# Optimization experiments

Measured on AMD Instinct MI355X. Metric: run time of the kernel, lower is better.

## Reference

```python
import jax, jax.numpy as jnp
import numpy as np

B, T, C = 2, 2048, 1024
H, GAMMA = 16, 8
D = C // H
SCALE = 1.0 / np.sqrt(D).astype(np.float32)


def setup_inputs() -> dict:
    key = jax.random.key(0)
    ks = jax.random.split(key, 6)
    w = 0.02
    return {
        'x': jax.random.normal(ks[0], (B, T, C), dtype=jnp.float32),
        'Wq': jax.random.normal(ks[1], (C, 2 * C), dtype=jnp.float32) * w,
        'Wk': jax.random.normal(ks[2], (C, 2 * C), dtype=jnp.float32) * w,
        'Wv': jax.random.normal(ks[3], (C, C), dtype=jnp.float32) * w,
        'Wo': jax.random.normal(ks[4], (C, C), dtype=jnp.float32) * w,
        'theta_offset': jax.random.normal(ks[5], (H,), dtype=jnp.float32) * 0.1,
    }


def _heads(t):
    # (B, T, C) -> (B, H, T, D)
    return t.reshape(B, T, H, D).transpose(0, 2, 1, 3)


def reference(x, Wq, Wk, Wv, Wo, theta_offset):
    q_raw = x @ Wq                      # (B, T, 2C)
    k_raw = x @ Wk                      # (B, T, 2C)
    v = _heads(x @ Wv)                  # (B, H, T, D)

    q_amp, q_phase = jnp.split(q_raw, 2, axis=-1)
    k_amp, k_phase = jnp.split(k_raw, 2, axis=-1)
    q_amp = jax.nn.softplus(_heads(q_amp))
    q_phase = _heads(q_phase)
    k_amp = jax.nn.softplus(_heads(k_amp))
    k_phase = _heads(k_phase)

    q_real = q_amp * jnp.cos(q_phase)
    q_imag = q_amp * jnp.sin(q_phase)
    k_real = k_amp * jnp.cos(k_phase)
    k_imag = k_amp * jnp.sin(k_phase)

    scores = (jnp.einsum('bhtd,bhsd->bhts', q_real, k_real)
              + jnp.einsum('bhtd,bhsd->bhts', q_imag, k_imag)) * SCALE

    # theta gating (active since T > GAMMA)
    cycle_ids = jnp.arange(T, dtype=jnp.float32) / GAMMA
    cycle_dist = cycle_ids[None, :] - cycle_ids[:, None]        # (T, T)
    theta_gate = jnp.cos(theta_offset[:, None, None] * cycle_dist)  # (H, T, T)
    scores = scores * theta_gate[None]

    causal = jnp.tril(jnp.ones((T, T), dtype=bool))
    scores = jnp.where(causal[None, None], scores, -jnp.inf)
    attn = jax.nn.softmax(scores, axis=-1)

    out = jnp.einsum('bhts,bhsd->bhtd', attn, v)
    out = out.transpose(0, 2, 1, 3).reshape(B, T, C)
    return out @ Wo
```

## Files before the change

### kernel.cpp

```cpp
#include <hip/hip_runtime.h>
#include <hip/hip_bf16.h>
#include <math.h>

#define Bc 2
#define Tc 2048
#define Cc 1024
#define Hc 16
#define Dc 64

typedef __attribute__((ext_vector_type(8))) short short8;
typedef __attribute__((ext_vector_type(4))) float f32x4;

#define L2E 1.44269504088896f
#define SM_M 20.0f

__device__ __forceinline__ short f2bf(float x) {
    unsigned u = __float_as_uint(x);
    u += 0x7fff + ((u >> 16) & 1);
    return (short)(u >> 16);
}
__device__ __forceinline__ unsigned pack2bf_fast(float a, float b) {
    unsigned ua = __float_as_uint(a) + 0x8000u;
    unsigned ub = __float_as_uint(b) + 0x8000u;
    return __builtin_amdgcn_perm(ub, ua, 0x07060302);
}
__device__ __forceinline__ float softplus_fast(float a) {
    return fmaxf(a, 0.f) + __logf(1.f + __expf(-fabsf(a)));
}

#define RDA(BUF, MH) do {                                                      \
    const short* Ah_ = &Al[BUF][MH][0];                                        \
    _Pragma("unroll") for (int mt_ = 0; mt_ < 4; ++mt_) {                      \
        af[mt_][0] = *(const short8*)&Ah_[(wm*64 + mt_*16 + c)*64 + rsw0];     \
        af[mt_][1] = *(const short8*)&Ah_[(wm*64 + mt_*16 + c)*64 + rsw1];     \
    } } while (0)

#define RDB(BUF, NH) do {                                                      \
    const short* Bh_ = &Bl[BUF][NH][0];                                        \
    _Pragma("unroll") for (int nf_ = 0; nf_ < 2; ++nf_) {                      \
        bfr[NH][nf_][0] = *(const short8*)&Bh_[(wn*32 + nf_*16 + c)*64 + rsw0];\
        bfr[NH][nf_][1] = *(const short8*)&Bh_[(wn*32 + nf_*16 + c)*64 + rsw1];\
    } } while (0)

#define MMQ(MH, NH) do {                                                       \
    _Pragma("unroll") for (int mt_ = 0; mt_ < 4; ++mt_)                        \
    _Pragma("unroll") for (int nf_ = 0; nf_ < 2; ++nf_) {                      \
        acc[MH][NH][mt_][nf_] = __builtin_amdgcn_mfma_f32_16x16x32_bf16(       \
            af[mt_][0], bfr[NH][nf_][0], acc[MH][NH][mt_][nf_], 0, 0, 0);      \
        acc[MH][NH][mt_][nf_] = __builtin_amdgcn_mfma_f32_16x16x32_bf16(       \
            af[mt_][1], bfr[NH][nf_][1], acc[MH][NH][mt_][nf_], 0, 0, 0);      \
    } } while (0)

#define BARw asm volatile("s_barrier" ::: "memory")
#define VMW6 asm volatile("s_waitcnt vmcnt(6)" ::: "memory")
#define VMW0 asm volatile("s_waitcnt vmcnt(0)" ::: "memory")
#define PRIO1 __builtin_amdgcn_s_setprio(1)
#define PRIO0 __builtin_amdgcn_s_setprio(0)

__global__ __launch_bounds__(512, 2) void gemm256_qk(
    const short* __restrict__ A, const short* __restrict__ Bt,
    short* __restrict__ q2, short* __restrict__ k2)
{
    __shared__ __attribute__((aligned(16))) short Al[2][2][128 * 64];
    __shared__ __attribute__((aligned(16))) short Bl[2][2][128 * 64];

    const int tid = threadIdx.x;
    const int wave = tid >> 6, lane = tid & 63;
    const int quad = lane >> 4, c = lane & 15;
    const int wm = wave >> 2, wn = wave & 3;
    const int f = blockIdx.x + 16 * blockIdx.y;
    const int w = (f & 7) * 32 + (f >> 3);
    const int bx = w & 15, by = w >> 4;
    const int m0 = by * 256, n0 = bx * 256;

    const int rsw0 = ((quad * 16) ^ ((c & 7) << 4)) >> 1;
    const int rsw1 = ((64 + quad * 16) ^ ((c & 7) << 4)) >> 1;

    f32x4 acc[2][2][4][2];
#pragma unroll
    for (int a0 = 0; a0 < 2; ++a0)
#pragma unroll
        for (int a1 = 0; a1 < 2; ++a1)
#pragma unroll
            for (int a2 = 0; a2 < 4; ++a2)
#pragma unroll
                for (int a3 = 0; a3 < 2; ++a3)
                    acc[a0][a1][a2][a3] = (f32x4){0.f, 0.f, 0.f, 0.f};

    short8 af[4][2];
    short8 bfr[2][2][2];

    auto stA = [&](int kt, int hh) {
        short* dstb = &Al[kt & 1][hh][0];
#pragma unroll
        for (int j = 0; j < 2; ++j) {
            int ch = j * 512 + tid;
            int row = ch >> 3;
            int os = ((((ch & 7) << 4) ^ ((row & 7) << 4)) >> 1);
            const short* src = A + (size_t)(m0 + hh * 128 + row) * 1024 + kt * 64 + os;
            __builtin_amdgcn_global_load_lds(
                (const __attribute__((address_space(1))) void*)src,
                (__attribute__((address_space(3))) void*)(dstb + (j * 512 + wave * 64) * 8),
                16, 0, 0);
        }
    };
    auto stB = [&](int kt, int hh) {
        short* dstb = &Bl[kt & 1][hh][0];
#pragma unroll
        for (int j = 0; j < 2; ++j) {
            int ch = j * 512 + tid;
            int row = ch >> 3;
            int os = ((((ch & 7) << 4) ^ ((row & 7) << 4)) >> 1);
            const short* src = Bt + (size_t)(n0 + hh * 128 + row) * 1024 + kt * 64 + os;
            __builtin_amdgcn_global_load_lds(
                (const __attribute__((address_space(1))) void*)src,
                (__attribute__((address_space(3))) void*)(dstb + (j * 512 + wave * 64) * 8),
                16, 0, 0);
        }
    };

    stB(0, 0); stA(0, 0); stB(0, 1); stA(0, 1); stB(1, 0); stA(1, 0); stB(1, 1);
    VMW6;
    BARw;

    for (int i = 0; i < 8; ++i) {
        const int e = 2 * i;
        const bool more = (i < 7);
        RDA(0, 0); RDB(0, 0);
        stA(e + 1, 1);
        BARw; PRIO1; MMQ(0, 0); PRIO0; BARw;
        RDB(0, 1);
        if (more) stB(e + 2, 0);
        BARw; PRIO1; MMQ(0, 1); PRIO0; BARw;
        RDA(0, 1);
        if (more) stA(e + 2, 0);
        BARw; PRIO1; MMQ(1, 0); PRIO0; BARw;
        if (more) stB(e + 2, 1);
        BARw; PRIO1; MMQ(1, 1); PRIO0;
        if (more) { VMW6; } else { VMW0; }
        BARw;
        RDA(1, 0); RDB(1, 0);
        if (more) stA(e + 2, 1);
        BARw; PRIO1; MMQ(0, 0); PRIO0; BARw;
        RDB(1, 1);
        if (more) stB(e + 3, 0);
        BARw; PRIO1; MMQ(0, 1); PRIO0; BARw;
        RDA(1, 1);
        if (more) stA(e + 3, 0);
        BARw; PRIO1; MMQ(1, 0); PRIO0; BARw;
        if (more) stB(e + 3, 1);
        BARw; PRIO1; MMQ(1, 1); PRIO0;
        if (more) { VMW6; } else { VMW0; }
        BARw;
    }

    const int d = wn * 16 + c;
#pragma unroll
    for (int mh = 0; mh < 2; ++mh) {
#pragma unroll
        for (int nh = 0; nh < 2; ++nh) {
            const int g = 2 * bx + nh;
            const int isK = g >> 4;
            const int hh = g & 15;
            const float scl = isK ? 1.f : 0.125f;
            short* dst = isK ? k2 : q2;
#pragma unroll
            for (int mt = 0; mt < 4; ++mt) {
#pragma unroll
                for (int reg = 0; reg < 4; ++reg) {
                    int m = m0 + mh * 128 + wm * 64 + mt * 16 + quad * 4 + reg;
                    int bb = m >> 11, tt = m & (Tc - 1);
                    size_t base = (((size_t)bb * Hc + hh) * Tc + tt) * 128;
                    float amp = acc[mh][nh][mt][0][reg];
                    float ph  = acc[mh][nh][mt][1][reg];
                    float sp = softplus_fast(amp) * scl;
                    float sn, cs;
                    __sincosf(ph, &sn, &cs);
                    dst[base + d]      = f2bf(sp * cs);
                    dst[base + d + 64] = f2bf(sp * sn);
                }
            }
        }
    }
}

template <int EPI>
__global__ __launch_bounds__(512) void gemm_bt_mfma(
    const short* __restrict__ A, const short* __restrict__ Bt,
    float* __restrict__ Cf, short* __restrict__ Cb,
    int M, int N, int K)
{
    __shared__ __attribute__((aligned(16))) short As[128 * 32];
    __shared__ __attribute__((aligned(16))) short Bs[128 * 32];

    const int tid = threadIdx.x;
    const int lane = tid & 63;
    const int wave = tid >> 6;
    const int quad = lane >> 4, c = lane & 15;
    const int wm = wave >> 1, wn = wave & 1;
    const int m0 = blockIdx.y * 128, n0 = blockIdx.x * 128;

    const int srow = tid >> 2;
    const int scol = (tid & 3) * 8;
    const short* Ag = A  + (size_t)(m0 + srow) * K + scol;
    const short* Bg = Bt + (size_t)(n0 + srow) * K + scol;
    short* AsW = As + tid * 8;
    short* BsW = Bs + tid * 8;

    f32x4 acc[2][4];
#pragma unroll
    for (int i = 0; i < 2; ++i)
#pragma unroll
        for (int j = 0; j < 4; ++j)
            acc[i][j] = (f32x4){0.f, 0.f, 0.f, 0.f};

    for (int k0 = 0; k0 < K; k0 += 32) {
        __syncthreads();
        __builtin_amdgcn_global_load_lds(
            (const __attribute__((address_space(1))) void*)(Ag + k0),
            (__attribute__((address_space(3))) void*)AsW, 16, 0, 0);
        __builtin_amdgcn_global_load_lds(
            (const __attribute__((address_space(1))) void*)(Bg + k0),
            (__attribute__((address_space(3))) void*)BsW, 16, 0, 0);
        __syncthreads();

        short8 af[2], bf[4];
#pragma unroll
        for (int mt = 0; mt < 2; ++mt)
            af[mt] = *(const short8*)&As[(wm * 32 + mt * 16 + c) * 32 + quad * 8];
#pragma unroll
        for (int nt = 0; nt < 4; ++nt)
            bf[nt] = *(const short8*)&Bs[(wn * 64 + nt * 16 + c) * 32 + quad * 8];
#pragma unroll
        for (int mt = 0; mt < 2; ++mt)
#pragma unroll
            for (int nt = 0; nt < 4; ++nt)
                acc[mt][nt] = __builtin_amdgcn_mfma_f32_16x16x32_bf16(
                    af[mt], bf[nt], acc[mt][nt], 0, 0, 0);
    }

#pragma unroll
    for (int mt = 0; mt < 2; ++mt) {
#pragma unroll
        for (int reg = 0; reg < 4; ++reg) {
            size_t row = m0 + wm * 32 + mt * 16 + quad * 4 + reg;
#pragma unroll
            for (int nt = 0; nt < 4; ++nt) {
                size_t col = n0 + wn * 64 + nt * 16 + c;
                if (EPI == 1) Cb[row * N + col] = f2bf(acc[mt][nt][reg]);
                else          Cf[row * N + col] = acc[mt][nt][reg];
            }
        }
    }
}

__global__ __launch_bounds__(512) void gemm_v2t(
    const short* __restrict__ A, const short* __restrict__ Bt,
    short* __restrict__ v2t)
{
    __shared__ __attribute__((aligned(16))) short As[128 * 32];
    __shared__ __attribute__((aligned(16))) short Bs[128 * 32];
    __shared__ __attribute__((aligned(16))) short tile[128 * 136];

    const int K = Cc;
    const int tid = threadIdx.x;
    const int lane = tid & 63;
    const int wave = tid >> 6;
    const int quad = lane >> 4, c = lane & 15;
    const int wm = wave >> 1, wn = wave & 1;
    const int m0 = blockIdx.y * 128, n0 = blockIdx.x * 128;

    const int srow = tid >> 2;
    const int scol = (tid & 3) * 8;
    const short* Ag = A  + (size_t)(m0 + srow) * K + scol;
    const short* Bg = Bt + (size_t)(n0 + srow) * K + scol;
    short* AsW = As + tid * 8;
    short* BsW = Bs + tid * 8;

    f32x4 acc[2][4];
#pragma unroll
    for (int i = 0; i < 2; ++i)
#pragma unroll
        for (int j = 0; j < 4; ++j)
            acc[i][j] = (f32x4){0.f, 0.f, 0.f, 0.f};

    for (int k0 = 0; k0 < K; k0 += 32) {
        __syncthreads();
        __builtin_amdgcn_global_load_lds(
            (const __attribute__((address_space(1))) void*)(Ag + k0),
            (__attribute__((address_space(3))) void*)AsW, 16, 0, 0);
        __builtin_amdgcn_global_load_lds(
            (const __attribute__((address_space(1))) void*)(Bg + k0),
            (__attribute__((address_space(3))) void*)BsW, 16, 0, 0);
        __syncthreads();

        short8 af[2], bf[4];
#pragma unroll
        for (int mt = 0; mt < 2; ++mt)
            af[mt] = *(const short8*)&As[(wm * 32 + mt * 16 + c) * 32 + quad * 8];
#pragma unroll
        for (int nt = 0; nt < 4; ++nt)
            bf[nt] = *(const short8*)&Bs[(wn * 64 + nt * 16 + c) * 32 + quad * 8];
#pragma unroll
        for (int mt = 0; mt < 2; ++mt)
#pragma unroll
            for (int nt = 0; nt < 4; ++nt)
                acc[mt][nt] = __builtin_amdgcn_mfma_f32_16x16x32_bf16(
                    af[mt], bf[nt], acc[mt][nt], 0, 0, 0);
    }

#pragma unroll
    for (int mt = 0; mt < 2; ++mt)
#pragma unroll
        for (int reg = 0; reg < 4; ++reg) {
            int tl = wm * 32 + mt * 16 + quad * 4 + reg;
#pragma unroll
            for (int nt = 0; nt < 4; ++nt)
                tile[(wn * 64 + nt * 16 + c) * 136 + tl] = f2bf(acc[mt][nt][reg]);
        }
    __syncthreads();

    const int b = m0 >> 11, tl0 = m0 & (Tc - 1);
#pragma unroll
    for (int i = 0; i < 4; ++i) {
        int n = i * 32 + (tid >> 4);
        int t8 = (tid & 15) * 8;
        int ng = n0 + n, h = ng >> 6, d = ng & 63;
        *(short8*)&v2t[(((size_t)b * Hc + h) * Dc + d) * Tc + tl0 + t8] =
            *(const short8*)&tile[n * 136 + t8];
    }
}

__global__ __launch_bounds__(256) void xconv(const float* __restrict__ x,
                                             short* __restrict__ xb)
{
    int idx = blockIdx.x * 256 + threadIdx.x;
    float4 v = *(const float4*)&x[(size_t)idx * 4];
    short4 o = {f2bf(v.x), f2bf(v.y), f2bf(v.z), f2bf(v.w)};
    *(short4*)&xb[(size_t)idx * 4] = o;
}

__global__ __launch_bounds__(256) void wtrans_qk(const float* __restrict__ Wq,
                                                 const float* __restrict__ Wk,
                                                 short* __restrict__ Bt)
{
    __shared__ short tile[64][80];
    const int n0 = blockIdx.x * 64, k0 = blockIdx.y * 64;
    const int half = blockIdx.z;
    const float* W = half ? Wk : Wq;
    const int tid = threadIdx.x;
#pragma unroll
    for (int i = 0; i < 4; ++i) {
        int e = i * 256 + tid;
        int k = e >> 4, n4 = (e & 15) * 4;
        float4 v = *(const float4*)&W[(size_t)(k0 + k) * 2048 + n0 + n4];
        tile[k][n4]     = f2bf(v.x);
        tile[k][n4 + 1] = f2bf(v.y);
        tile[k][n4 + 2] = f2bf(v.z);
        tile[k][n4 + 3] = f2bf(v.w);
    }
    __syncthreads();
#pragma unroll
    for (int i = 0; i < 16; ++i) {
        int e = i * 256 + tid;
        int n = e >> 6, k = e & 63;
        int ng = n0 + n;
        int sub = ng >> 10, hh = (ng >> 6) & 15, dd = ng & 63;
        int r = (half * 16 + hh) * 128 + (dd >> 4) * 32 + sub * 16 + (dd & 15);
        Bt[(size_t)r * Cc + k0 + k] = tile[k][n];
    }
}

__global__ __launch_bounds__(256) void wtrans2(const float* __restrict__ Wv,
                                               const float* __restrict__ Wo,
                                               short* __restrict__ WtBase)
{
    __shared__ short tile[64][80];
    const int n0 = blockIdx.x * 64, k0 = blockIdx.y * 64;
    const float* W = blockIdx.z ? Wo : Wv;
    short* Wt = WtBase + (size_t)blockIdx.z * Cc * Cc;
    const int tid = threadIdx.x;
#pragma unroll
    for (int i = 0; i < 4; ++i) {
        int e = i * 256 + tid;
        int k = e >> 4, n4 = (e & 15) * 4;
        float4 v = *(const float4*)&W[(size_t)(k0 + k) * Cc + n0 + n4];
        tile[k][n4]     = f2bf(v.x);
        tile[k][n4 + 1] = f2bf(v.y);
        tile[k][n4 + 2] = f2bf(v.z);
        tile[k][n4 + 3] = f2bf(v.w);
    }
    __syncthreads();
#pragma unroll
    for (int i = 0; i < 16; ++i) {
        int e = i * 256 + tid;
        int n = e >> 6, k = e & 63;
        Wt[(size_t)(n0 + n) * Cc + k0 + k] = tile[k][n];
    }
}

__global__ __launch_bounds__(512, 4) void moire_attn8(
    const short* __restrict__ q2, const short* __restrict__ k2,
    const short* __restrict__ v2t, const float* __restrict__ theta,
    short* __restrict__ att)
{
    __shared__ __attribute__((aligned(16))) short Ks[2][64 * 128];
    __shared__ __attribute__((aligned(16))) short Vt[2][64 * 64];
    __shared__ __attribute__((aligned(16))) short Ps[8][16 * 64];

    const int tid = threadIdx.x;
    const int wave = tid >> 6, lane = tid & 63;
    const int quad = lane >> 4, c = lane & 15;
    const int tx = wave >> 2, gw = wave & 3;
    const int f = blockIdx.x + 16 * (blockIdx.y + 16 * blockIdx.z);
    const int w = (f & 7) * 64 + (f >> 3);
    const int p = w & 15;
    const int hb = w >> 4;
    const int h = hb & 15, b = hb >> 4;
    const int qB = 31 - p;
    const float th = theta[h];

    const short* k2b = k2 + (size_t)(b * Hc + h) * Tc * 128;
    const short* v2b = v2t + (size_t)(b * Hc + h) * Dc * Tc;
    const short* q2b = q2 + (size_t)(b * Hc + h) * Tc * 128;

    int qcur = tx ? qB : p;
    int q0 = qcur * 64;
    const int t_l = gw * 16 + c;

    short8 qf[4];
    {
        const short* qp = q2b + (size_t)(q0 + t_l) * 128;
#pragma unroll
        for (int i = 0; i < 4; ++i)
            qf[i] = *(const short8*)(qp + i * 32 + quad * 8);
    }

    float x0 = th * 0.125f * (float)(q0 + t_l);
    float cb = __cosf(x0), sb = -__sinf(x0);
    float cOff[4][4], sOff[4][4];
#pragma unroll
    for (int mt = 0; mt < 4; ++mt)
#pragma unroll
        for (int reg = 0; reg < 4; ++reg) {
            float a = th * 0.125f * (float)(mt * 16 + quad * 4 + reg);
            cOff[mt][reg] = __cosf(a) * L2E;
            sOff[mt][reg] = __sinf(a) * L2E;
        }
    const float cD = __cosf(8.f * th), sD = __sinf(8.f * th);

    f32x4 oacc[4];
    float lsum = 0.f;
#pragma unroll
    for (int nt = 0; nt < 4; ++nt)
        oacc[nt] = (f32x4){0.f, 0.f, 0.f, 0.f};

    auto stageK_all = [&](int jts, int buf) {
        short* dst = &Ks[buf][0];
        const int s0 = jts * 64;
#pragma unroll
        for (int i = 0; i < 2; ++i) {
            int ch = i * 512 + tid;
            int row = ch >> 4, j = ch & 15;
            const short* src = k2b + (size_t)(s0 + row) * 128 + ((j ^ (row & 15)) << 3);
            __builtin_amdgcn_global_load_lds(
                (const __attribute__((address_space(1))) void*)src,
                (__attribute__((address_space(3))) void*)(dst + (i * 512 + wave * 64) * 8),
                16, 0, 0);
        }
    };
    auto stageV_all = [&](int jts, int buf) {
        short* dst = &Vt[buf][0];
        const int s0 = jts * 64;
        int row = tid >> 3, j = tid & 7;
        const short* src = v2b + (size_t)row * Tc + s0 + ((j ^ (row & 7)) << 3);
        __builtin_amdgcn_global_load_lds(
            (const __attribute__((address_space(1))) void*)src,
            (__attribute__((address_space(3))) void*)(dst + (wave * 64) * 8),
            16, 0, 0);
    };
    auto stage_grp = [&](int jts, int buf) {
        const int s0 = jts * 64;
        const int ltid = tid & 255;
        short* dk = &Ks[buf][0];
#pragma unroll
        for (int jj = 0; jj < 4; ++jj) {
            int ch = jj * 256 + ltid;
            int row = ch >> 4, j = ch & 15;
            const short* src = k2b + (size_t)(s0 + row) * 128 + ((j ^ (row & 15)) << 3);
            __builtin_amdgcn_global_load_lds(
                (const __attribute__((address_space(1))) void*)src,
                (__attribute__((address_space(3))) void*)(dk + (jj * 256 + gw * 64) * 8),
                16, 0, 0);
        }
        short* dv = &Vt[buf][0];
#pragma unroll
        for (int jj = 0; jj < 2; ++jj) {
            int ch = jj * 256 + ltid;
            int row = ch >> 3, j = ch & 7;
            const short* src = v2b + (size_t)row * Tc + s0 + ((j ^ (row & 7)) << 3);
            __builtin_amdgcn_global_load_lds(
                (const __attribute__((address_space(1))) void*)src,
                (__attribute__((address_space(3))) void*)(dv + (jj * 256 + gw * 64) * 8),
                16, 0, 0);
        }
    };

    auto do_s = [&](int jt, int buf) {
        const short* KsB = &Ks[buf][0];
        const bool diag = (jt == qcur);

        f32x4 s_acc[4];
#pragma unroll
        for (int mt = 0; mt < 4; ++mt) {
            f32x4 a = {0.f, 0.f, 0.f, 0.f};
#pragma unroll
            for (int kk = 0; kk < 4; ++kk) {
                short8 kf = *(const short8*)&KsB[(mt * 16 + c) * 128 +
                                                 (((kk * 4 + quad) ^ c) << 3)];
                a = __builtin_amdgcn_mfma_f32_16x16x32_bf16(kf, qf[kk], a, 0, 0, 0);
            }
            s_acc[mt] = a;
        }

#pragma unroll
        for (int mt = 0; mt < 4; ++mt) {
            float pv[4];
#pragma unroll
            for (int reg = 0; reg < 4; ++reg) {
                float g2 = cb * cOff[mt][reg] - sb * sOff[mt][reg];
                float arg = fmaf(s_acc[mt][reg], g2, -SM_M * L2E);
                if (diag && (mt * 16 + quad * 4 + reg) > t_l) arg = -1e30f;
                pv[reg] = exp2f(arg);
            }
            lsum += (pv[0] + pv[1]) + (pv[2] + pv[3]);
            uint2 pk = {pack2bf_fast(pv[0], pv[1]), pack2bf_fast(pv[2], pv[3])};
            int slot = ((mt * 2 + (quad >> 1)) ^ (c & 7));
            *(uint2*)&Ps[wave][c * 64 + slot * 8 + (quad & 1) * 4] = pk;
        }

        float ncb = cb * cD - sb * sD;
        sb = sb * cD + cb * sD;
        cb = ncb;
    };

    auto do_pv = [&](int buf) {
        const short* VtB = &Vt[buf][0];
        short8 pf[2];
#pragma unroll
        for (int kk = 0; kk < 2; ++kk)
            pf[kk] = *(const short8*)&Ps[wave][c * 64 +
                         (((kk * 4 + quad) ^ (c & 7)) << 3)];
#pragma unroll
        for (int nt = 0; nt < 4; ++nt)
#pragma unroll
            for (int kk = 0; kk < 2; ++kk) {
                short8 vf = *(const short8*)&VtB[(nt * 16 + c) * 64 +
                             (((kk * 4 + quad) ^ (c & 7)) << 3)];
                oacc[nt] = __builtin_amdgcn_mfma_f32_16x16x32_bf16(
                    pf[kk], vf, oacc[nt], 0, 0, 0);
            }
    };

    auto write_out = [&]() {
        float l = lsum;
        l += __shfl_xor(l, 16);
        l += __shfl_xor(l, 32);
        float il = 1.f / l;
        float ilr[4];
#pragma unroll
        for (int reg = 0; reg < 4; ++reg)
            ilr[reg] = __shfl(il, quad * 4 + reg);
#pragma unroll
        for (int reg = 0; reg < 4; ++reg) {
            int t_o = q0 + gw * 16 + quad * 4 + reg;
#pragma unroll
            for (int nt = 0; nt < 4; ++nt)
                att[(size_t)(b * Tc + t_o) * Cc + h * Dc + nt * 16 + c] =
                    f2bf(oacc[nt][reg] * ilr[reg]);
        }
    };

    stageK_all(0, 0); stageV_all(0, 0);
    for (int jt = 0; jt <= p; ++jt) {
        __syncthreads();
        stageK_all(jt + 1, (jt + 1) & 1);
        stageV_all(jt + 1, (jt + 1) & 1);
        do_s(jt, jt & 1);
        do_pv(jt & 1);
    }
    const int slotB = (p + 1) & 1, slotA = slotB ^ 1;

    __syncthreads();
    if (tx == 0) {
        write_out();
#pragma unroll
        for (int nt = 0; nt < 4; ++nt)
            oacc[nt] = (f32x4){0.f, 0.f, 0.f, 0.f};
        lsum = 0.f;
        qcur = qB; q0 = qB * 64;
        const short* qp = q2b + (size_t)(q0 + t_l) * 128;
#pragma unroll
        for (int i = 0; i < 4; ++i)
            qf[i] = *(const short8*)(qp + i * 32 + quad * 8);
        float a = th * 0.125f * (1088.f - (float)(q0 + t_l));
        __sincosf(a, &sb, &cb);
    } else {
        do_s(p + 1, slotB);
        do_pv(slotB);
    }

    for (int i = 0; i <= 14 - p; ++i) {
        const int jt = tx ? (p + 2 + i) : (17 + i);
        const int sl = tx ? slotB : slotA;
        __syncthreads();
        stage_grp(jt, sl);
        __syncthreads();
        do_s(jt, sl);
        do_pv(sl);
    }

    __syncthreads();
    float* Cmb = (float*)&Ks[0][0];
    if (tx == 0) {
        float* pp = Cmb + (size_t)(gw * 64 + lane) * 20;
#pragma unroll
        for (int nt = 0; nt < 4; ++nt) *(f32x4*)(pp + nt * 4) = oacc[nt];
        pp[16] = lsum;
    }
    __syncthreads();
    if (tx == 1) {
        const float* pp = Cmb + (size_t)(gw * 64 + lane) * 20;
#pragma unroll
        for (int nt = 0; nt < 4; ++nt)
            oacc[nt] += *(const f32x4*)(pp + nt * 4);
        lsum += pp[16];
        write_out();
    }
}

extern "C" void kernel_launch(void* const* d_in, const int* in_sizes, int n_in,
                              void* d_out, int out_size, void* d_ws, size_t ws_size,
                              hipStream_t stream)
{
    const float* x     = (const float*)d_in[0];
    const float* Wq    = (const float*)d_in[1];
    const float* Wk    = (const float*)d_in[2];
    const float* Wv    = (const float*)d_in[3];
    const float* Wo    = (const float*)d_in[4];
    const float* theta = (const float*)d_in[5];
    float* out = (float*)d_out;

    const int M = Bc * Tc;
    char* ws = (char*)d_ws;
    const size_t MB = 1 << 20;
    short* xb   = (short*)(ws);
    short* Bqk  = (short*)(ws + 8 * MB);
    short* Wvt  = (short*)(ws + 16 * MB);
    short* Wot  = (short*)(ws + 18 * MB);
    short* v2t  = (short*)(ws + 28 * MB);
    short* attb = (short*)(ws + 36 * MB);
    short* q2   = (short*)(ws + 44 * MB);
    short* k2   = (short*)d_out;

    xconv<<<(size_t)M * Cc / 1024, 256, 0, stream>>>(x, xb);
    wtrans_qk<<<dim3(2048 / 64, Cc / 64, 2), 256, 0, stream>>>(Wq, Wk, Bqk);
    wtrans2<<<dim3(Cc / 64, Cc / 64, 2), 256, 0, stream>>>(Wv, Wo, Wvt);

    gemm256_qk<<<dim3(4096 / 256, M / 256), 512, 0, stream>>>(xb, Bqk, q2, k2);
    gemm_v2t<<<dim3(Cc / 128, M / 128), 512, 0, stream>>>(xb, Wvt, v2t);

    moire_attn8<<<dim3(16, Hc, Bc), 512, 0, stream>>>(q2, k2, v2t, theta, attb);

    gemm_bt_mfma<0><<<dim3(Cc / 128, M / 128), 512, 0, stream>>>(
        attb, Wot, out, nullptr, M, Cc, Cc);
}
```

Measured before the change: 232.2 us.

## Prefetch K/V tiles into registers during split-group attention phase

In the second phase where the two wave-groups process different key tiles, the synchronous global-to-LDS staging is replaced by a register prefetch: the next tile's K and V are loaded into registers while the current tile is computed, then written to LDS at the start of the next iteration. This is meant to hide global load latency that previously sat between two barriers. The causal-mask check is also split into a diagonal and a non-diagonal code path so off-diagonal tiles skip the per-element compare. It costs extra VGPRs for the prefetch buffers, which may pressure occupancy under the 512x4 launch bounds.

```diff
diff --git a/kernel.cpp b/kernel.cpp
--- a/kernel.cpp
+++ b/kernel.cpp
@@ -399,7 +399,7 @@
     }
 }
 
-__global__ __launch_bounds__(512, 4) void moire_attn8(
+__global__ __launch_bounds__(512, 4) void moire_attn9(
     const short* __restrict__ q2, const short* __restrict__ k2,
     const short* __restrict__ v2t, const float* __restrict__ theta,
     short* __restrict__ att)
@@ -479,36 +479,39 @@
             (__attribute__((address_space(3))) void*)(dst + (wave * 64) * 8),
             16, 0, 0);
     };
-    auto stage_grp = [&](int jts, int buf) {
+
+    short8 rK[4], rV[2];
+    const int ltid = tid & 255;
+    auto pf_load = [&](int jts) {
         const int s0 = jts * 64;
-        const int ltid = tid & 255;
-        short* dk = &Ks[buf][0];
 #pragma unroll
         for (int jj = 0; jj < 4; ++jj) {
             int ch = jj * 256 + ltid;
             int row = ch >> 4, j = ch & 15;
-            const short* src = k2b + (size_t)(s0 + row) * 128 + ((j ^ (row & 15)) << 3);
-            __builtin_amdgcn_global_load_lds(
-                (const __attribute__((address_space(1))) void*)src,
-                (__attribute__((address_space(3))) void*)(dk + (jj * 256 + gw * 64) * 8),
-                16, 0, 0);
-        }
-        short* dv = &Vt[buf][0];
+            rK[jj] = *(const short8*)(k2b + (size_t)(s0 + row) * 128 +
+                                      ((j ^ (row & 15)) << 3));
+        }
 #pragma unroll
         for (int jj = 0; jj < 2; ++jj) {
             int ch = jj * 256 + ltid;
             int row = ch >> 3, j = ch & 7;
-            const short* src = v2b + (size_t)row * Tc + s0 + ((j ^ (row & 7)) << 3);
-            __builtin_amdgcn_global_load_lds(
-                (const __attribute__((address_space(1))) void*)src,
-                (__attribute__((address_space(3))) void*)(dv + (jj * 256 + gw * 64) * 8),
-                16, 0, 0);
-        }
+            rV[jj] = *(const short8*)(v2b + (size_t)row * Tc + s0 +
+                                      ((j ^ (row & 7)) << 3));
+        }
+    };
+    auto pf_write = [&](int buf) {
+        short* dk = &Ks[buf][0];
+        short* dv = &Vt[buf][0];
+#pragma unroll
+        for (int jj = 0; jj < 4; ++jj)
+            *(short8*)(dk + (jj * 256 + ltid) * 8) = rK[jj];
+#pragma unroll
+        for (int jj = 0; jj < 2; ++jj)
+            *(short8*)(dv + (jj * 256 + ltid) * 8) = rV[jj];
     };
 
     auto do_s = [&](int jt, int buf) {
         const short* KsB = &Ks[buf][0];
-        const bool diag = (jt == qcur);
 
         f32x4 s_acc[4];
 #pragma unroll
@@ -523,20 +526,37 @@
             s_acc[mt] = a;
         }
 
-#pragma unroll
-        for (int mt = 0; mt < 4; ++mt) {
-            float pv[4];
-#pragma unroll
-            for (int reg = 0; reg < 4; ++reg) {
-                float g2 = cb * cOff[mt][reg] - sb * sOff[mt][reg];
-                float arg = fmaf(s_acc[mt][reg], g2, -SM_M * L2E);
-                if (diag && (mt * 16 + quad * 4 + reg) > t_l) arg = -1e30f;
-                pv[reg] = exp2f(arg);
+        if (jt == qcur) {
+#pragma unroll
+            for (int mt = 0; mt < 4; ++mt) {
+                float pv[4];
+#pragma unroll
+                for (int reg = 0; reg < 4; ++reg) {
+                    float g2 = cb * cOff[mt][reg] - sb * sOff[mt][reg];
+                    float arg = fmaf(s_acc[mt][reg], g2, -SM_M * L2E);
+                    if ((mt * 16 + quad * 4 + reg) > t_l) arg = -1e30f;
+                    pv[reg] = exp2f(arg);
+                }
+                lsum += (pv[0] + pv[1]) + (pv[2] + pv[3]);
+                uint2 pk = {pack2bf_fast(pv[0], pv[1]), pack2bf_fast(pv[2], pv[3])};
+                int slot = ((mt * 2 + (quad >> 1)) ^ (c & 7));
+                *(uint2*)&Ps[wave][c * 64 + slot * 8 + (quad & 1) * 4] = pk;
             }
-            lsum += (pv[0] + pv[1]) + (pv[2] + pv[3]);
-            uint2 pk = {pack2bf_fast(pv[0], pv[1]), pack2bf_fast(pv[2], pv[3])};
-            int slot = ((mt * 2 + (quad >> 1)) ^ (c & 7));
-            *(uint2*)&Ps[wave][c * 64 + slot * 8 + (quad & 1) * 4] = pk;
+        } else {
+#pragma unroll
+            for (int mt = 0; mt < 4; ++mt) {
+                float pv[4];
+#pragma unroll
+                for (int reg = 0; reg < 4; ++reg) {
+                    float g2 = cb * cOff[mt][reg] - sb * sOff[mt][reg];
+                    float arg = fmaf(s_acc[mt][reg], g2, -SM_M * L2E);
+                    pv[reg] = exp2f(arg);
+                }
+                lsum += (pv[0] + pv[1]) + (pv[2] + pv[3]);
+                uint2 pk = {pack2bf_fast(pv[0], pv[1]), pack2bf_fast(pv[2], pv[3])};
+                int slot = ((mt * 2 + (quad >> 1)) ^ (c & 7));
+                *(uint2*)&Ps[wave][c * 64 + slot * 8 + (quad & 1) * 4] = pk;
+            }
         }
 
         float ncb = cb * cD - sb * sD;
@@ -592,6 +612,7 @@
     const int slotB = (p + 1) & 1, slotA = slotB ^ 1;
 
     __syncthreads();
+    if (p < 15) pf_load(tx ? (p + 2) : 17);
     if (tx == 0) {
         write_out();
 #pragma unroll
@@ -614,8 +635,9 @@
         const int jt = tx ? (p + 2 + i) : (17 + i);
         const int sl = tx ? slotB : slotA;
         __syncthreads();
-        stage_grp(jt, sl);
+        pf_write(sl);
         __syncthreads();
+        if (i < 14 - p) pf_load(jt + 1);
         do_s(jt, sl);
         do_pv(sl);
     }
@@ -670,7 +692,7 @@
     gemm256_qk<<<dim3(4096 / 256, M / 256), 512, 0, stream>>>(xb, Bqk, q2, k2);
     gemm_v2t<<<dim3(Cc / 128, M / 128), 512, 0, stream>>>(xb, Wvt, v2t);
 
-    moire_attn8<<<dim3(16, Hc, Bc), 512, 0, stream>>>(q2, k2, v2t, theta, attb);
+    moire_attn9<<<dim3(16, Hc, Bc), 512, 0, stream>>>(q2, k2, v2t, theta, attb);
 
     gemm_bt_mfma<0><<<dim3(Cc / 128, M / 128), 512, 0, stream>>>(
         attb, Wot, out, nullptr, M, Cc, Cc);
```

Result: slower. 410.6 us (+76.8%).
